# Optimization experiments

Hardware: AMD Instinct MI355X
Metric: run time of the kernel (lower is better)

## Reference

```python
import jax, jax.numpy as jnp
import numpy as np

N_NODES = 100000
N_EDGES = 1600000
DIM = 128
N_LAYERS = 3
BN_EPS = 1e-5


def setup_inputs() -> dict:
    key = jax.random.key(0)
    ks = jax.random.split(key, 8)
    x = jax.random.normal(ks[0], (N_NODES, DIM), dtype=jnp.float32)
    edge_index = jax.random.randint(ks[1], (2, N_EDGES), 0, N_NODES, dtype=jnp.int64)
    # Stacked per-layer params (all layers are DIM->DIM since input_dim==hidden_dim)
    W1 = jax.random.normal(ks[2], (N_LAYERS, DIM, DIM), dtype=jnp.float32) * 0.05
    b1 = jnp.zeros((N_LAYERS, DIM), dtype=jnp.float32)
    gamma = jnp.ones((N_LAYERS, DIM), dtype=jnp.float32)
    beta = jnp.zeros((N_LAYERS, DIM), dtype=jnp.float32)
    rmean = jnp.zeros((N_LAYERS, DIM), dtype=jnp.float32)
    rvar = jnp.ones((N_LAYERS, DIM), dtype=jnp.float32)
    W2 = jax.random.normal(ks[3], (N_LAYERS, DIM, DIM), dtype=jnp.float32) * 0.05
    b2 = jnp.zeros((N_LAYERS, DIM), dtype=jnp.float32)
    return {"x": x, "edge_index": edge_index, "W1": W1, "b1": b1,
            "gamma": gamma, "beta": beta, "rmean": rmean, "rvar": rvar,
            "W2": W2, "b2": b2}


def _gin_layer(h, src, dst, W1_l, b1_l, g_l, be_l, m_l, v_l, W2_l, b2_l):
    # adj_t @ h : sum of neighbor (src) features into dst nodes
    agg = jax.ops.segment_sum(h[src], dst, num_segments=N_NODES)
    h = h + agg  # (1 + eps) * x + agg, eps = 0
    h = h @ W1_l + b1_l
    # BatchNorm1d (inference mode, running stats)
    h = (h - m_l) * jax.lax.rsqrt(v_l + BN_EPS) * g_l + be_l
    h = jax.nn.relu(h)
    h = h @ W2_l + b2_l
    return jax.nn.relu(h)


def reference(x, edge_index, W1, b1, gamma, beta, rmean, rvar, W2, b2):
    src, dst = edge_index[0], edge_index[1]
    h = x
    for l in range(N_LAYERS):
        h = _gin_layer(h, src, dst, W1[l], b1[l], gamma[l], beta[l],
                       rmean[l], rvar[l], W2[l], b2[l])
        # dropout is identity in eval mode
    return jax.nn.log_softmax(h, axis=-1)
```

## Files before the change

kernel.cpp:

```cpp
#include <hip/hip_runtime.h>
#include <hip/hip_bf16.h>
#include <cstdint>

#define DIM 128
#define ASTR 136
#define WSTR 136
#define NBKT 512
#define BCAP 4608
#define ECHUNK 2500

typedef __bf16 bf16x8 __attribute__((ext_vector_type(8)));
typedef float  f32x4  __attribute__((ext_vector_type(4)));
typedef unsigned short u16x8 __attribute__((ext_vector_type(8)));
typedef unsigned short u16x4 __attribute__((ext_vector_type(4)));

__device__ __forceinline__ unsigned short f2bf(float f) {
    union { float f; unsigned u; } x; x.f = f;
    unsigned r = x.u + 0x7fffu + ((x.u >> 16) & 1u);
    return (unsigned short)(r >> 16);
}
__device__ __forceinline__ float2 bfpair2f(unsigned v) {
    union { unsigned u; float f; } a, b;
    a.u = v << 16;
    b.u = v & 0xffff0000u;
    return make_float2(a.f, b.f);
}

__device__ __forceinline__ void load_edge(const unsigned* __restrict__ eidx,
                                          int e, int E, int is64,
                                          int& s, int& d) {
    if (is64) {
        s = (int)eidx[2 * (size_t)e];
        d = (int)eidx[2 * ((size_t)E + (size_t)e)];
    } else {
        s = (int)eidx[(size_t)e];
        d = (int)eidx[(size_t)E + (size_t)e];
    }
}

__global__ __launch_bounds__(256) void prep_all(
    const float* __restrict__ x,
    const float* __restrict__ W1, const float* __restrict__ W2,
    const float* __restrict__ b1, const float* __restrict__ g,
    const float* __restrict__ be, const float* __restrict__ m,
    const float* __restrict__ v, const unsigned* __restrict__ eidx,
    unsigned short* __restrict__ Wt, float* __restrict__ affA,
    float* __restrict__ affB, u16x4* __restrict__ P,
    int* __restrict__ flag, int* __restrict__ gpos,
    int M, int xblk, int wblk)
{
    const int b = blockIdx.x, t = threadIdx.x;
    if (b < xblk) {
        int id = b * 256 + t;
        if (id < M * 32) {
            float4 vv = ((const float4*)x)[id];
            u16x4 o;
            o[0] = f2bf(vv.x); o[1] = f2bf(vv.y);
            o[2] = f2bf(vv.z); o[3] = f2bf(vv.w);
            P[id] = o;
        }
    } else if (b < xblk + wblk) {
        int id = (b - xblk) * 256 + t;
        int l = id / 32768;
        int r = id - l * 32768;
        int w = r >> 14;
        int idx = r & 16383;
        int k = idx >> 7, n = idx & 127;
        const float* src = (w ? W2 : W1) + (size_t)l * 16384;
        Wt[(size_t)id - idx + ((size_t)n * 128 + k)] = f2bf(src[k * 128 + n]);
    } else {
        for (int id = t; id < 3 * DIM; id += 256) {
            float A = g[id] * rsqrtf(v[id] + 1e-5f);
            affA[id] = A;
            affB[id] = (b1[id] - m[id]) * A + be[id];
        }
        for (int id = t; id < NBKT; id += 256) gpos[id] = 0;
        if (t == 0) {
            int is64 = 1;
            for (int i = 0; i < 32; ++i)
                if (eidx[2 * i + 1] != 0u) { is64 = 0; break; }
            *flag = is64;
        }
    }
}

__global__ __launch_bounds__(256) void bin_edges(
    const unsigned* __restrict__ eidx, int E, const int* __restrict__ flag,
    int* __restrict__ gpos, unsigned* __restrict__ binned)
{
    __shared__ int cnt[NBKT];
    __shared__ int bas[NBKT];
    __shared__ unsigned pk[ECHUNK];
    __shared__ unsigned short bkL[ECHUNK];
    const int t = threadIdx.x;
    const int e0 = blockIdx.x * ECHUNK;
    int n = E - e0; if (n > ECHUNK) n = ECHUNK;
    const int is64 = *flag;

    for (int i = t; i < NBKT; i += 256) cnt[i] = 0;
    __syncthreads();
    for (int i = t; i < n; i += 256) {
        int s, d; load_edge(eidx, e0 + i, E, is64, s, d);
        int bk = d >> 8;
        pk[i] = ((unsigned)s << 8) | (unsigned)(d & 255);
        bkL[i] = (unsigned short)bk;
        atomicAdd(&cnt[bk], 1);
    }
    __syncthreads();
    for (int i = t; i < NBKT; i += 256) {
        int c = cnt[i];
        bas[i] = c ? atomicAdd(&gpos[i], c) : 0;
    }
    __syncthreads();
    for (int i = t; i < n; i += 256) {
        int bk = bkL[i];
        int slot = atomicAdd(&bas[bk], 1);
        if (slot < BCAP)
            binned[(size_t)bk * BCAP + slot] = pk[i];
    }
}

__global__ __launch_bounds__(256) void bucket_fill(
    const unsigned* __restrict__ binned, const int* __restrict__ gpos,
    int* __restrict__ off, int* __restrict__ csr, int M)
{
    __shared__ int sc[NBKT];
    __shared__ int cntL[256];
    __shared__ int sh[256];
    __shared__ int posL[256];
    const int b = blockIdx.x;
    const int t = threadIdx.x;

    sc[t]       = min(gpos[t], BCAP);
    sc[t + 256] = min(gpos[t + 256], BCAP);
    __syncthreads();
    for (int ofs = 1; ofs < NBKT; ofs <<= 1) {
        int a0 = (t >= ofs) ? sc[t - ofs] : 0;
        int a1 = sc[t + 256 - ofs];
        __syncthreads();
        sc[t] += a0; sc[t + 256] += a1;
        __syncthreads();
    }
    const int nb   = min(gpos[b], BCAP);
    const int base = sc[b] - nb;

    cntL[t] = 0;
    __syncthreads();
    for (int i = t; i < nb; i += 256)
        atomicAdd(&cntL[binned[(size_t)b * BCAP + i] & 255], 1);
    __syncthreads();
    sh[t] = cntL[t];
    __syncthreads();
    #pragma unroll
    for (int ofs = 1; ofs < 256; ofs <<= 1) {
        int add = (t >= ofs) ? sh[t - ofs] : 0;
        __syncthreads();
        sh[t] += add;
        __syncthreads();
    }
    int excl = sh[t] - cntL[t];
    int node = b * 256 + t;
    if (node <= M) off[node] = base + excl;
    posL[t] = excl;
    __syncthreads();
    for (int i = t; i < nb; i += 256) {
        unsigned vv = binned[(size_t)b * BCAP + i];
        int slot = atomicAdd(&posL[vv & 255], 1);
        csr[base + slot] = (int)(vv >> 8);
    }
}

__device__ __forceinline__ void addpair(float2& a, unsigned v) {
    float2 p = bfpair2f(v);
    a.x += p.x; a.y += p.y;
}

__global__ __launch_bounds__(256) void gather_v(
    const uint4* __restrict__ Hv,
    const int* __restrict__ off, const int* __restrict__ csr,
    uint4* __restrict__ AGv, int M)
{
    int node = (blockIdx.x * 256 + threadIdx.x) >> 6;
    if (node >= M) return;
    int lane = threadIdx.x & 63;
    int q = lane >> 4, li = lane & 15;

    float2 acc[4];
    acc[0] = acc[1] = acc[2] = acc[3] = make_float2(0.f, 0.f);
    if (q == 0) {
        uint4 w = Hv[(size_t)node * 16 + li];
        acc[0] = bfpair2f(w.x); acc[1] = bfpair2f(w.y);
        acc[2] = bfpair2f(w.z); acc[3] = bfpair2f(w.w);
    }

    const int beg = off[node], end = off[node + 1];
    for (int jb = beg; jb < end; jb += 32) {
        int idx[8];
        uint4 w[8];
        #pragma unroll
        for (int u = 0; u < 8; ++u) {
            idx[u] = jb + u * 4 + q;
            int ic = idx[u] < end ? idx[u] : end - 1;
            int s = csr[ic];
            w[u] = Hv[(size_t)s * 16 + li];
        }
        #pragma unroll
        for (int u = 0; u < 8; ++u) {
            if (idx[u] >= end) { w[u].x = 0; w[u].y = 0; w[u].z = 0; w[u].w = 0; }
            addpair(acc[0], w[u].x);
            addpair(acc[1], w[u].y);
            addpair(acc[2], w[u].z);
            addpair(acc[3], w[u].w);
        }
    }

    #pragma unroll
    for (int k = 0; k < 4; ++k) {
        acc[k].x += __shfl_xor(acc[k].x, 16);
        acc[k].y += __shfl_xor(acc[k].y, 16);
        acc[k].x += __shfl_xor(acc[k].x, 32);
        acc[k].y += __shfl_xor(acc[k].y, 32);
    }
    if (q == 0) {
        uint4 o;
        o.x = (unsigned)f2bf(acc[0].x) | ((unsigned)f2bf(acc[0].y) << 16);
        o.y = (unsigned)f2bf(acc[1].x) | ((unsigned)f2bf(acc[1].y) << 16);
        o.z = (unsigned)f2bf(acc[2].x) | ((unsigned)f2bf(acc[2].y) << 16);
        o.w = (unsigned)f2bf(acc[3].x) | ((unsigned)f2bf(acc[3].y) << 16);
        AGv[(size_t)node * 16 + li] = o;
    }
}

template<int LAST>
__global__ __launch_bounds__(256) void fused_layer(
    const unsigned short* __restrict__ AGGb,
    const unsigned short* __restrict__ W1t,
    const unsigned short* __restrict__ W2t,
    const float* __restrict__ affA, const float* __restrict__ affB,
    const float* __restrict__ b2, void* __restrict__ OUTp, int M)
{
    __shared__ unsigned short Asub[64 * ASTR];
    __shared__ unsigned short Wsub[128 * WSTR];
    const int t = threadIdx.x;
    const int row0 = blockIdx.x * 64;
    const int w = t >> 6;
    const int lane = t & 63;
    const int lm = lane & 15;
    const int quad = lane >> 4;

    #pragma unroll
    for (int i = 0; i < 4; ++i) {
        int idx = t + 256 * i;
        int row = idx >> 4, ch = idx & 15;
        int gr = row0 + row;
        u16x8 v = {0, 0, 0, 0, 0, 0, 0, 0};
        if (gr < M) v = ((const u16x8*)(AGGb + (size_t)gr * DIM))[ch];
        *(u16x8*)&Asub[row * ASTR + ch * 8] = v;
    }
    #pragma unroll
    for (int i = 0; i < 16; ++i) {
        int idx = t + 256 * i;
        int n = idx >> 5, kc = idx & 31;
        *(ushort4*)&Wsub[n * WSTR + kc * 4] = ((const ushort4*)W1t)[idx];
    }
    __syncthreads();

    const int arow = w * 16 + lm;
    f32x4 acc[8];
    #pragma unroll
    for (int i = 0; i < 8; ++i) { f32x4 z = {0.f, 0.f, 0.f, 0.f}; acc[i] = z; }
    #pragma unroll
    for (int kc = 0; kc < 4; ++kc) {
        int k0 = kc * 32 + quad * 8;
        bf16x8 a = *(const bf16x8*)&Asub[arow * ASTR + k0];
        #pragma unroll
        for (int tt = 0; tt < 8; ++tt) {
            bf16x8 b = *(const bf16x8*)&Wsub[(tt * 16 + lm) * WSTR + k0];
            acc[tt] = __builtin_amdgcn_mfma_f32_16x16x32_bf16(a, b, acc[tt], 0, 0, 0);
        }
    }

    #pragma unroll
    for (int tt = 0; tt < 8; ++tt) {
        int c = tt * 16 + lm;
        float aA = affA[c], aB = affB[c];
        #pragma unroll
        for (int r = 0; r < 4; ++r) {
            float h = fmaxf(acc[tt][r] * aA + aB, 0.f);
            Asub[(w * 16 + quad * 4 + r) * ASTR + c] = f2bf(h);
        }
    }
    __syncthreads();
    #pragma unroll
    for (int i = 0; i < 16; ++i) {
        int idx = t + 256 * i;
        int n = idx >> 5, kc = idx & 31;
        *(ushort4*)&Wsub[n * WSTR + kc * 4] = ((const ushort4*)W2t)[idx];
    }
    __syncthreads();

    f32x4 acc2[8];
    #pragma unroll
    for (int i = 0; i < 8; ++i) { f32x4 z = {0.f, 0.f, 0.f, 0.f}; acc2[i] = z; }
    #pragma unroll
    for (int kc = 0; kc < 4; ++kc) {
        int k0 = kc * 32 + quad * 8;
        bf16x8 a = *(const bf16x8*)&Asub[arow * ASTR + k0];
        #pragma unroll
        for (int tt = 0; tt < 8; ++tt) {
            bf16x8 b = *(const bf16x8*)&Wsub[(tt * 16 + lm) * WSTR + k0];
            acc2[tt] = __builtin_amdgcn_mfma_f32_16x16x32_bf16(a, b, acc2[tt], 0, 0, 0);
        }
    }

    float v[8][4];
    #pragma unroll
    for (int tt = 0; tt < 8; ++tt) {
        int c = tt * 16 + lm;
        float bb = b2[c];
        #pragma unroll
        for (int r = 0; r < 4; ++r)
            v[tt][r] = fmaxf(acc2[tt][r] + bb, 0.f);
    }

    if (!LAST) {
        unsigned short* OUT = (unsigned short*)OUTp;
        #pragma unroll
        for (int tt = 0; tt < 8; ++tt) {
            int c = tt * 16 + lm;
            #pragma unroll
            for (int r = 0; r < 4; ++r) {
                int gr = row0 + w * 16 + quad * 4 + r;
                if (gr < M) OUT[(size_t)gr * DIM + c] = f2bf(v[tt][r]);
            }
        }
    } else {
        float* OUT = (float*)OUTp;
        #pragma unroll
        for (int r = 0; r < 4; ++r) {
            float mm = v[0][r];
            #pragma unroll
            for (int tt = 1; tt < 8; ++tt) mm = fmaxf(mm, v[tt][r]);
            #pragma unroll
            for (int ofs = 1; ofs < 16; ofs <<= 1)
                mm = fmaxf(mm, __shfl_xor(mm, ofs));
            float ss = 0.f;
            #pragma unroll
            for (int tt = 0; tt < 8; ++tt) ss += __expf(v[tt][r] - mm);
            #pragma unroll
            for (int ofs = 1; ofs < 16; ofs <<= 1)
                ss += __shfl_xor(ss, ofs);
            float lse = mm + __logf(ss);
            int gr = row0 + w * 16 + quad * 4 + r;
            if (gr < M) {
                #pragma unroll
                for (int tt = 0; tt < 8; ++tt)
                    OUT[(size_t)gr * DIM + tt * 16 + lm] = v[tt][r] - lse;
            }
        }
    }
}

static inline size_t align256(size_t v) { return (v + 255) & ~(size_t)255; }

extern "C" void kernel_launch(void* const* d_in, const int* in_sizes, int n_in,
                              void* d_out, int out_size, void* d_ws, size_t ws_size,
                              hipStream_t stream) {
    const float*    x     = (const float*)d_in[0];
    const unsigned* eidx  = (const unsigned*)d_in[1];
    const float*    W1    = (const float*)d_in[2];
    const float*    b1    = (const float*)d_in[3];
    const float*    gamma = (const float*)d_in[4];
    const float*    beta  = (const float*)d_in[5];
    const float*    rmean = (const float*)d_in[6];
    const float*    rvar  = (const float*)d_in[7];
    const float*    W2    = (const float*)d_in[8];
    const float*    b2    = (const float*)d_in[9];

    const int M = in_sizes[0] / DIM;
    const int E = in_sizes[1] / 2;
    const size_t hbf_bytes = (size_t)M * DIM * 2;

    float* out = (float*)d_out;
    char*  ws  = (char*)d_ws;

    size_t o = 0;
    int* flag = (int*)(ws + o);                     o = align256(o + 4);
    unsigned short* Wt = (unsigned short*)(ws + o); o = align256(o + (size_t)3 * 2 * 16384 * 2);
    float* affA = (float*)(ws + o);                 o = align256(o + 3 * DIM * 4);
    float* affB = (float*)(ws + o);                 o = align256(o + 3 * DIM * 4);
    int* gpos  = (int*)(ws + o);                    o = align256(o + NBKT * 4);
    int* off   = (int*)(ws + o);                    o = align256(o + ((size_t)M + 1) * 4);
    int* csr   = (int*)(ws + o);                    o = align256(o + (size_t)E * 4);
    unsigned short* P = (unsigned short*)(ws + o);  o = align256(o + hbf_bytes);
    unsigned short* Q = (unsigned short*)(ws + o);  o = align256(o + hbf_bytes);
    unsigned* binned = (unsigned*)Q;

    const int xblk = (M * 32 + 255) / 256;
    const int wblk = (3 * 2 * 16384 + 255) / 256;
    prep_all<<<xblk + wblk + 1, 256, 0, stream>>>(
        x, W1, W2, b1, gamma, beta, rmean, rvar, eidx,
        Wt, affA, affB, (u16x4*)P, flag, gpos, M, xblk, wblk);

    const int bblk = (E + ECHUNK - 1) / ECHUNK;
    bin_edges<<<bblk, 256, 0, stream>>>(eidx, E, flag, gpos, binned);
    bucket_fill<<<NBKT, 256, 0, stream>>>(binned, gpos, off, csr, M);

    const int gat_blocks  = (M + 3) / 4;
    const int fuse_blocks = (M + 63) / 64;

    gather_v<<<gat_blocks, 256, 0, stream>>>((const uint4*)P, off, csr,
                                             (uint4*)Q, M);
    fused_layer<0><<<fuse_blocks, 256, 0, stream>>>(
        Q, Wt + 0 * 16384, Wt + 1 * 16384,
        affA + 0 * DIM, affB + 0 * DIM, b2 + 0 * DIM, (void*)P, M);
    gather_v<<<gat_blocks, 256, 0, stream>>>((const uint4*)P, off, csr,
                                             (uint4*)Q, M);
    fused_layer<0><<<fuse_blocks, 256, 0, stream>>>(
        Q, Wt + 2 * 16384, Wt + 3 * 16384,
        affA + 1 * DIM, affB + 1 * DIM, b2 + 1 * DIM, (void*)P, M);
    gather_v<<<gat_blocks, 256, 0, stream>>>((const uint4*)P, off, csr,
                                             (uint4*)Q, M);
    fused_layer<1><<<fuse_blocks, 256, 0, stream>>>(
        Q, Wt + 4 * 16384, Wt + 5 * 16384,
        affA + 2 * DIM, affB + 2 * DIM, b2 + 2 * DIM, (void*)out, M);
}
```

Measured before the change: 419.6 us.

## Fuse edge binning into prep kernel, stage buckets in LDS, load A fragments directly

```diff
diff --git a/kernel.cpp b/kernel.cpp
--- a/kernel.cpp
+++ b/kernel.cpp
@@ -38,7 +38,7 @@
     }
 }
 
-__global__ __launch_bounds__(256) void prep_all(
+__global__ __launch_bounds__(256) void prep_bin(
     const float* __restrict__ x,
     const float* __restrict__ W1, const float* __restrict__ W2,
     const float* __restrict__ b1, const float* __restrict__ g,
@@ -46,12 +46,46 @@
     const float* __restrict__ v, const unsigned* __restrict__ eidx,
     unsigned short* __restrict__ Wt, float* __restrict__ affA,
     float* __restrict__ affB, u16x4* __restrict__ P,
-    int* __restrict__ flag, int* __restrict__ gpos,
-    int M, int xblk, int wblk)
+    int* __restrict__ gpos, unsigned* __restrict__ binned,
+    int M, int E, int bblk, int xblk, int wblk)
 {
+    __shared__ int cnt[NBKT];
+    __shared__ int bas[NBKT];
+    __shared__ unsigned pk[ECHUNK];
+    __shared__ unsigned short bkL[ECHUNK];
     const int b = blockIdx.x, t = threadIdx.x;
-    if (b < xblk) {
-        int id = b * 256 + t;
+
+    if (b < bblk) {
+        int is64 = 1;
+        #pragma unroll 4
+        for (int i = 0; i < 32; ++i)
+            if (eidx[2 * i + 1] != 0u) { is64 = 0; break; }
+        const int e0 = b * ECHUNK;
+        int n = E - e0; if (n > ECHUNK) n = ECHUNK;
+
+        for (int i = t; i < NBKT; i += 256) cnt[i] = 0;
+        __syncthreads();
+        for (int i = t; i < n; i += 256) {
+            int s, d; load_edge(eidx, e0 + i, E, is64, s, d);
+            int bk = d >> 8;
+            pk[i] = ((unsigned)s << 8) | (unsigned)(d & 255);
+            bkL[i] = (unsigned short)bk;
+            atomicAdd(&cnt[bk], 1);
+        }
+        __syncthreads();
+        for (int i = t; i < NBKT; i += 256) {
+            int c = cnt[i];
+            bas[i] = c ? atomicAdd(&gpos[i], c) : 0;
+        }
+        __syncthreads();
+        for (int i = t; i < n; i += 256) {
+            int bk = bkL[i];
+            int slot = atomicAdd(&bas[bk], 1);
+            if (slot < BCAP)
+                binned[(size_t)bk * BCAP + slot] = pk[i];
+        }
+    } else if (b < bblk + xblk) {
+        int id = (b - bblk) * 256 + t;
         if (id < M * 32) {
             float4 vv = ((const float4*)x)[id];
             u16x4 o;
@@ -59,8 +93,8 @@
             o[2] = f2bf(vv.z); o[3] = f2bf(vv.w);
             P[id] = o;
         }
-    } else if (b < xblk + wblk) {
-        int id = (b - xblk) * 256 + t;
+    } else if (b < bblk + xblk + wblk) {
+        int id = (b - bblk - xblk) * 256 + t;
         int l = id / 32768;
         int r = id - l * 32768;
         int w = r >> 14;
@@ -74,49 +108,6 @@
             affA[id] = A;
             affB[id] = (b1[id] - m[id]) * A + be[id];
         }
-        for (int id = t; id < NBKT; id += 256) gpos[id] = 0;
-        if (t == 0) {
-            int is64 = 1;
-            for (int i = 0; i < 32; ++i)
-                if (eidx[2 * i + 1] != 0u) { is64 = 0; break; }
-            *flag = is64;
-        }
-    }
-}
-
-__global__ __launch_bounds__(256) void bin_edges(
-    const unsigned* __restrict__ eidx, int E, const int* __restrict__ flag,
-    int* __restrict__ gpos, unsigned* __restrict__ binned)
-{
-    __shared__ int cnt[NBKT];
-    __shared__ int bas[NBKT];
-    __shared__ unsigned pk[ECHUNK];
-    __shared__ unsigned short bkL[ECHUNK];
-    const int t = threadIdx.x;
-    const int e0 = blockIdx.x * ECHUNK;
-    int n = E - e0; if (n > ECHUNK) n = ECHUNK;
-    const int is64 = *flag;
-
-    for (int i = t; i < NBKT; i += 256) cnt[i] = 0;
-    __syncthreads();
-    for (int i = t; i < n; i += 256) {
-        int s, d; load_edge(eidx, e0 + i, E, is64, s, d);
-        int bk = d >> 8;
-        pk[i] = ((unsigned)s << 8) | (unsigned)(d & 255);
-        bkL[i] = (unsigned short)bk;
-        atomicAdd(&cnt[bk], 1);
-    }
-    __syncthreads();
-    for (int i = t; i < NBKT; i += 256) {
-        int c = cnt[i];
-        bas[i] = c ? atomicAdd(&gpos[i], c) : 0;
-    }
-    __syncthreads();
-    for (int i = t; i < n; i += 256) {
-        int bk = bkL[i];
-        int slot = atomicAdd(&bas[bk], 1);
-        if (slot < BCAP)
-            binned[(size_t)bk * BCAP + slot] = pk[i];
     }
 }
 
@@ -124,6 +115,7 @@
     const unsigned* __restrict__ binned, const int* __restrict__ gpos,
     int* __restrict__ off, int* __restrict__ csr, int M)
 {
+    __shared__ unsigned bl[BCAP];
     __shared__ int sc[NBKT];
     __shared__ int cntL[256];
     __shared__ int sh[256];
@@ -133,6 +125,7 @@
 
     sc[t]       = min(gpos[t], BCAP);
     sc[t + 256] = min(gpos[t + 256], BCAP);
+    const int nb = min(gpos[b], BCAP);
     __syncthreads();
     for (int ofs = 1; ofs < NBKT; ofs <<= 1) {
         int a0 = (t >= ofs) ? sc[t - ofs] : 0;
@@ -141,13 +134,14 @@
         sc[t] += a0; sc[t + 256] += a1;
         __syncthreads();
     }
-    const int nb   = min(gpos[b], BCAP);
     const int base = sc[b] - nb;
 
+    for (int i = t; i < nb; i += 256)
+        bl[i] = binned[(size_t)b * BCAP + i];
     cntL[t] = 0;
     __syncthreads();
     for (int i = t; i < nb; i += 256)
-        atomicAdd(&cntL[binned[(size_t)b * BCAP + i] & 255], 1);
+        atomicAdd(&cntL[bl[i] & 255], 1);
     __syncthreads();
     sh[t] = cntL[t];
     __syncthreads();
@@ -164,7 +158,7 @@
     posL[t] = excl;
     __syncthreads();
     for (int i = t; i < nb; i += 256) {
-        unsigned vv = binned[(size_t)b * BCAP + i];
+        unsigned vv = bl[i];
         int slot = atomicAdd(&posL[vv & 255], 1);
         csr[base + slot] = (int)(vv >> 8);
     }
@@ -239,7 +233,7 @@
     const float* __restrict__ affA, const float* __restrict__ affB,
     const float* __restrict__ b2, void* __restrict__ OUTp, int M)
 {
-    __shared__ unsigned short Asub[64 * ASTR];
+    __shared__ unsigned short H1s[64 * ASTR];
     __shared__ unsigned short Wsub[128 * WSTR];
     const int t = threadIdx.x;
     const int row0 = blockIdx.x * 64;
@@ -248,15 +242,12 @@
     const int lm = lane & 15;
     const int quad = lane >> 4;
 
-    #pragma unroll
-    for (int i = 0; i < 4; ++i) {
-        int idx = t + 256 * i;
-        int row = idx >> 4, ch = idx & 15;
-        int gr = row0 + row;
-        u16x8 v = {0, 0, 0, 0, 0, 0, 0, 0};
-        if (gr < M) v = ((const u16x8*)(AGGb + (size_t)gr * DIM))[ch];
-        *(u16x8*)&Asub[row * ASTR + ch * 8] = v;
-    }
+    const unsigned short* ap = AGGb + (size_t)(row0 + w * 16 + lm) * DIM;
+    bf16x8 afr[4];
+    #pragma unroll
+    for (int kc = 0; kc < 4; ++kc)
+        afr[kc] = *(const bf16x8*)(ap + kc * 32 + quad * 8);
+
     #pragma unroll
     for (int i = 0; i < 16; ++i) {
         int idx = t + 256 * i;
@@ -265,14 +256,13 @@
     }
     __syncthreads();
 
-    const int arow = w * 16 + lm;
     f32x4 acc[8];
     #pragma unroll
     for (int i = 0; i < 8; ++i) { f32x4 z = {0.f, 0.f, 0.f, 0.f}; acc[i] = z; }
     #pragma unroll
     for (int kc = 0; kc < 4; ++kc) {
         int k0 = kc * 32 + quad * 8;
-        bf16x8 a = *(const bf16x8*)&Asub[arow * ASTR + k0];
+        bf16x8 a = afr[kc];
         #pragma unroll
         for (int tt = 0; tt < 8; ++tt) {
             bf16x8 b = *(const bf16x8*)&Wsub[(tt * 16 + lm) * WSTR + k0];
@@ -287,7 +277,7 @@
         #pragma unroll
         for (int r = 0; r < 4; ++r) {
             float h = fmaxf(acc[tt][r] * aA + aB, 0.f);
-            Asub[(w * 16 + quad * 4 + r) * ASTR + c] = f2bf(h);
+            H1s[(w * 16 + quad * 4 + r) * ASTR + c] = f2bf(h);
         }
     }
     __syncthreads();
@@ -299,13 +289,14 @@
     }
     __syncthreads();
 
+    const int arow = w * 16 + lm;
     f32x4 acc2[8];
     #pragma unroll
     for (int i = 0; i < 8; ++i) { f32x4 z = {0.f, 0.f, 0.f, 0.f}; acc2[i] = z; }
     #pragma unroll
     for (int kc = 0; kc < 4; ++kc) {
         int k0 = kc * 32 + quad * 8;
-        bf16x8 a = *(const bf16x8*)&Asub[arow * ASTR + k0];
+        bf16x8 a = *(const bf16x8*)&H1s[arow * ASTR + k0];
         #pragma unroll
         for (int tt = 0; tt < 8; ++tt) {
             bf16x8 b = *(const bf16x8*)&Wsub[(tt * 16 + lm) * WSTR + k0];
@@ -385,25 +376,24 @@
     char*  ws  = (char*)d_ws;
 
     size_t o = 0;
-    int* flag = (int*)(ws + o);                     o = align256(o + 4);
     unsigned short* Wt = (unsigned short*)(ws + o); o = align256(o + (size_t)3 * 2 * 16384 * 2);
     float* affA = (float*)(ws + o);                 o = align256(o + 3 * DIM * 4);
     float* affB = (float*)(ws + o);                 o = align256(o + 3 * DIM * 4);
     int* gpos  = (int*)(ws + o);                    o = align256(o + NBKT * 4);
     int* off   = (int*)(ws + o);                    o = align256(o + ((size_t)M + 1) * 4);
     int* csr   = (int*)(ws + o);                    o = align256(o + (size_t)E * 4);
+    unsigned short* Q = (unsigned short*)(ws + o);  o = align256(o + hbf_bytes);
     unsigned short* P = (unsigned short*)(ws + o);  o = align256(o + hbf_bytes);
-    unsigned short* Q = (unsigned short*)(ws + o);  o = align256(o + hbf_bytes);
     unsigned* binned = (unsigned*)Q;
 
+    const int bblk = (E + ECHUNK - 1) / ECHUNK;
     const int xblk = (M * 32 + 255) / 256;
     const int wblk = (3 * 2 * 16384 + 255) / 256;
-    prep_all<<<xblk + wblk + 1, 256, 0, stream>>>(
+
+    hipMemsetAsync(gpos, 0, NBKT * 4, stream);
+    prep_bin<<<bblk + xblk + wblk + 1, 256, 0, stream>>>(
         x, W1, W2, b1, gamma, beta, rmean, rvar, eidx,
-        Wt, affA, affB, (u16x4*)P, flag, gpos, M, xblk, wblk);
-
-    const int bblk = (E + ECHUNK - 1) / ECHUNK;
-    bin_edges<<<bblk, 256, 0, stream>>>(eidx, E, flag, gpos, binned);
+        Wt, affA, affB, (u16x4*)P, gpos, binned, M, E, bblk, xblk, wblk);
     bucket_fill<<<NBKT, 256, 0, stream>>>(binned, gpos, off, csr, M);
 
     const int gat_blocks  = (M + 3) / 4;
```

Measured after the change: 405.7 us. 1.03x faster.
